# Performance work log

Hardware: AMD Instinct MI355X
Metric: run time of the kernel (lower is better)

## Reference

```python
import jax, jax.numpy as jnp
import numpy as np
import math

E = 8          # num_experts (= max_expert_num)
M = 1024       # hidden_size
H = 4096       # expert FFN dim (4*hidden)
B, S = 4, 4096 # batch, seq
CAP_FACTOR = 1.0
MIN_CAPACITY = 4


def setup_inputs() -> dict:
    key = jax.random.key(0)
    ks = jax.random.split(key, 5)
    hidden_states = jax.random.normal(ks[0], (B, S, M), dtype=jnp.float32)
    wg = jax.random.normal(ks[1], (M, E), dtype=jnp.float32) * (M ** -0.5)  # gate Linear (no bias, as in TopKGate)
    w1 = jax.random.normal(ks[2], (E, M, H), dtype=jnp.float32) * (M ** -0.5)
    b1 = jnp.zeros((E, H), dtype=jnp.float32)
    w2 = jax.random.normal(ks[3], (E, H, M), dtype=jnp.float32) * (H ** -0.5)
    b2 = jnp.zeros((E, M), dtype=jnp.float32)
    return {"hidden_states": hidden_states, "wg": wg, "w1": w1, "b1": b1, "w2": w2, "b2": b2}


def reference(hidden_states, wg, w1, b1, w2, b2):
    b, s_len, m = hidden_states.shape
    x = hidden_states.reshape(-1, m)            # [s, m], s = tokens
    s = x.shape[0]
    capacity = max(int(math.ceil(s / E * CAP_FACTOR)), MIN_CAPACITY)  # static

    # ---- top-1 gating (DeepSpeed top1gating, fp32, no jitter, no RTS) ----
    logits = x.astype(jnp.float32) @ wg          # [s, e]
    gates = jax.nn.softmax(logits, axis=1)
    idx = jnp.argmax(gates, axis=1)              # chosen expert per token
    mask1 = jax.nn.one_hot(idx, E, dtype=jnp.float32)
    exp_counts = jnp.sum(mask1, axis=0).astype(jnp.int32)
    ce = jnp.mean(mask1, axis=0)                 # fraction routed per expert (pre-drop)
    me = jnp.mean(gates, axis=0)
    l_aux = jnp.sum(me * ce) * E                 # load-balancing loss

    # position of each token within its expert's queue; drop past capacity
    locations = jnp.cumsum(mask1, axis=0) - 1.0  # [s, e]
    loc = jnp.sum(locations * mask1, axis=1).astype(jnp.int32)  # [s]
    keep = (loc < capacity).astype(jnp.float32)  # capacity drop mask
    gate_s = jnp.sum(gates * mask1, axis=1) * keep
    loc_c = jnp.clip(loc, 0, capacity - 1)

    # ---- dispatch: scatter tokens to [E, C, M] slots (equiv. to einsum('sec,sm->ecm')) ----
    dispatched = jnp.zeros((E, capacity, m), dtype=x.dtype).at[idx, loc_c].add(x * keep[:, None])

    # ---- grouped expert GEMMs (MLP with GELU) ----
    h = jax.nn.gelu(jnp.einsum('ecm,emh->ech', dispatched, w1) + b1[:, None, :])
    eout = jnp.einsum('ech,ehm->ecm', h, w2) + b2[:, None, :]

    # ---- combine: gather back and scale by gate value (dropped tokens -> 0) ----
    out = eout[idx, loc_c] * gate_s[:, None]     # [s, m]
    return out.reshape(b, s_len, m), l_aux, exp_counts
```

## Files before the change

kernel.cpp:

```cpp
#include <hip/hip_runtime.h>
#include <hip/hip_bf16.h>

#define TOKENS 16384
#define MDIM   1024
#define HDIM   4096
#define HHALF  2048
#define NEXP   8
#define CAP    2048

typedef __attribute__((ext_vector_type(8))) short bf16x8;
typedef __attribute__((ext_vector_type(4))) float f32x4;

__device__ __forceinline__ short f2bf(float x) {
  unsigned u = __float_as_uint(x);
  unsigned r = (u + 0x7fffu + ((u >> 16) & 1u)) >> 16;
  return (short)r;
}

__device__ __forceinline__ float gelu_f(float x) {
  float u = 1.5957691216057308f * (x + 0.044715f * x * x * x);
  float e = __expf(u);
  return x * (1.f - 1.f / (e + 1.f));
}

__global__ __launch_bounds__(256) void gating_kernel(
    const float* __restrict__ x, const float* __restrict__ wg,
    int* __restrict__ idx, float* __restrict__ gate,
    float* __restrict__ mepart) {
  __shared__ float me_s[NEXP];
  int tid = threadIdx.x, wid = tid >> 6, lane = tid & 63;
  if (tid < NEXP) me_s[tid] = 0.f;
  __syncthreads();
  int t = blockIdx.x * 4 + wid;
  float acc[NEXP];
#pragma unroll
  for (int e = 0; e < NEXP; e++) acc[e] = 0.f;
  const float4* xr = (const float4*)(x + (size_t)t * MDIM);
#pragma unroll
  for (int j = 0; j < 4; j++) {
    float4 xv = xr[lane * 4 + j];
    int base = lane * 16 + j * 4;
    const float* xp = &xv.x;
#pragma unroll
    for (int i = 0; i < 4; i++) {
      float xi = xp[i];
      const float4* wr = (const float4*)(wg + (size_t)(base + i) * NEXP);
      float4 w0 = wr[0], w1 = wr[1];
      acc[0] += xi * w0.x; acc[1] += xi * w0.y; acc[2] += xi * w0.z; acc[3] += xi * w0.w;
      acc[4] += xi * w1.x; acc[5] += xi * w1.y; acc[6] += xi * w1.z; acc[7] += xi * w1.w;
    }
  }
#pragma unroll
  for (int off = 32; off > 0; off >>= 1)
#pragma unroll
    for (int e = 0; e < NEXP; e++) acc[e] += __shfl_xor(acc[e], off, 64);
  if (lane == 0) {
    float mx = acc[0]; int ai = 0;
#pragma unroll
    for (int e = 1; e < NEXP; e++) if (acc[e] > mx) { mx = acc[e]; ai = e; }
    float ex[NEXP]; float se = 0.f;
#pragma unroll
    for (int e = 0; e < NEXP; e++) { ex[e] = __expf(acc[e] - mx); se += ex[e]; }
    float inv = 1.f / se;
#pragma unroll
    for (int e = 0; e < NEXP; e++) atomicAdd(&me_s[e], ex[e] * inv);
    idx[t] = ai;
    gate[t] = inv;
  }
  __syncthreads();
  if (tid < NEXP) mepart[blockIdx.x * NEXP + tid] = me_s[tid];
}

__global__ __launch_bounds__(1024) void scan_kernel(
    const int* __restrict__ idx, float* __restrict__ gate,
    int* __restrict__ s2t, int* __restrict__ counts) {
  __shared__ int wcnt[16][NEXP];
  __shared__ int base[NEXP];
  int tid = threadIdx.x, wid = tid >> 6, lane = tid & 63;
  if (tid < NEXP) base[tid] = 0;
  __syncthreads();
  for (int chunk = 0; chunk < TOKENS; chunk += 1024) {
    int i = chunk + tid;
    int e = idx[i];
    int pre = 0;
#pragma unroll
    for (int e2 = 0; e2 < NEXP; e2++) {
      unsigned long long b = __ballot(e == e2);
      if (e2 == e) pre = __popcll(b & ((1ull << lane) - 1ull));
      if (lane == 0) wcnt[wid][e2] = __popcll(b);
    }
    __syncthreads();
    int off = base[e];
    for (int w = 0; w < wid; w++) off += wcnt[w][e];
    int loc = off + pre;
    if (loc < CAP) s2t[e * CAP + loc] = i;
    else           gate[i] = 0.f;
    __syncthreads();
    if (tid < NEXP) {
      int tsum = 0;
#pragma unroll
      for (int w = 0; w < 16; w++) tsum += wcnt[w][tid];
      base[tid] += tsum;
    }
    __syncthreads();
  }
  if (tid < NEXP) counts[tid] = base[tid];
}

__global__ __launch_bounds__(256) void finalize_kernel(
    const float* __restrict__ mepart, const int* __restrict__ counts,
    float* __restrict__ out_tail, int nblocks) {
  __shared__ float red[256];
  __shared__ float me[NEXP];
  int tid = threadIdx.x;
  float s = 0.f;
  int e = tid & 7;
  for (int r = tid >> 3; r < nblocks; r += 32) s += mepart[r * NEXP + e];
  red[tid] = s;
  __syncthreads();
  if (tid < NEXP) {
    float tsum = 0.f;
    for (int i = tid; i < 256; i += 8) tsum += red[i];
    me[tid] = tsum;
  }
  __syncthreads();
  if (tid == 0) {
    float la = 0.f;
    for (int k = 0; k < NEXP; k++)
      la += (me[k] / (float)TOKENS) * ((float)counts[k] / (float)TOKENS);
    out_tail[0] = la * (float)NEXP;
  }
  if (tid < NEXP) out_tail[1 + tid] = (float)counts[tid];
}

__global__ __launch_bounds__(256) void transpose_cvt_kernel(
    const float* __restrict__ in, short* __restrict__ out, int R, int Cc) {
  __shared__ float tile[32][33];
  int e = blockIdx.z;
  const float* in_e = in + (size_t)e * R * Cc;
  short* out_e = out + (size_t)e * R * Cc;
  int r0 = blockIdx.y * 32, c0 = blockIdx.x * 32;
  int tx = threadIdx.x & 31, ty = threadIdx.x >> 5;
#pragma unroll
  for (int i = 0; i < 4; i++)
    tile[ty + i * 8][tx] = in_e[(size_t)(r0 + ty + i * 8) * Cc + c0 + tx];
  __syncthreads();
#pragma unroll
  for (int i = 0; i < 4; i++)
    out_e[(size_t)(c0 + ty + i * 8) * R + r0 + tx] = f2bf(tile[tx][ty + i * 8]);
}

__global__ __launch_bounds__(256) void dispatch_kernel(
    const float* __restrict__ x, const int* __restrict__ s2t,
    short* __restrict__ A) {
  int slot = blockIdx.x;
  int token = s2t[slot];
  short4 v;
  if (token >= 0) {
    float4 xv = ((const float4*)(x + (size_t)token * MDIM))[threadIdx.x];
    v.x = f2bf(xv.x); v.y = f2bf(xv.y); v.z = f2bf(xv.z); v.w = f2bf(xv.w);
  } else {
    v.x = 0; v.y = 0; v.z = 0; v.w = 0;
  }
  ((short4*)(A + (size_t)slot * MDIM))[threadIdx.x] = v;
}

__device__ __forceinline__ void stage_tile(const short* __restrict__ g0, int ldk,
                                           short* lds, int tid) {
  int w = tid >> 6, lane = tid & 63;
#pragma unroll
  for (int i = 0; i < 4; i++) {
    int rbase = w * 32 + i * 8;
    int r = rbase + (lane >> 3);
    int c = (lane & 7) ^ (r & 7);
    const short* g = g0 + (size_t)r * ldk + c * 8;
    short* l = lds + rbase * 64;
    __builtin_amdgcn_global_load_lds((const __attribute__((address_space(1))) void*)g,
                                     (__attribute__((address_space(3))) void*)l,
                                     16, 0, 0);
  }
}

__global__ __launch_bounds__(256) void gemm1_kernel(
    const short* __restrict__ A, const short* __restrict__ Bt,
    const float* __restrict__ b1, short* __restrict__ Hh, int p) {
  __shared__ __align__(16) short ldsA[128 * 64];
  __shared__ __align__(16) short ldsB[128 * 64];
  int e = blockIdx.z, bm = blockIdx.y, bn = blockIdx.x;
  const short* Ae = A  + ((size_t)e * CAP  + (size_t)bm * 128) * MDIM;
  const short* Be = Bt + ((size_t)e * HDIM + (size_t)(p * HHALF + bn * 128)) * MDIM;
  int tid = threadIdx.x, lane = tid & 63, w = tid >> 6;
  int wr = (w >> 1) * 64, wc = (w & 1) * 64;
  f32x4 acc[4][4];
  f32x4 zero = {0.f, 0.f, 0.f, 0.f};
#pragma unroll
  for (int a = 0; a < 4; a++)
#pragma unroll
    for (int b = 0; b < 4; b++) acc[a][b] = zero;
  for (int kt = 0; kt < MDIM; kt += 64) {
    __syncthreads();
    stage_tile(Ae + kt, MDIM, ldsA, tid);
    stage_tile(Be + kt, MDIM, ldsB, tid);
    __syncthreads();
#pragma unroll
    for (int kk = 0; kk < 2; kk++) {
      bf16x8 af[4], bfr[4];
#pragma unroll
      for (int rt = 0; rt < 4; rt++) {
        int r = wr + rt * 16 + (lane & 15);
        int c = (kk * 4 + (lane >> 4)) ^ (r & 7);
        af[rt] = *(const bf16x8*)(ldsA + r * 64 + c * 8);
      }
#pragma unroll
      for (int ct = 0; ct < 4; ct++) {
        int r = wc + ct * 16 + (lane & 15);
        int c = (kk * 4 + (lane >> 4)) ^ (r & 7);
        bfr[ct] = *(const bf16x8*)(ldsB + r * 64 + c * 8);
      }
#pragma unroll
      for (int rt = 0; rt < 4; rt++)
#pragma unroll
        for (int ct = 0; ct < 4; ct++)
          acc[rt][ct] = __builtin_amdgcn_mfma_f32_16x16x32_bf16(af[rt], bfr[ct], acc[rt][ct], 0, 0, 0);
    }
  }
  int q = lane >> 4, ln = lane & 15;
#pragma unroll
  for (int ct = 0; ct < 4; ct++) {
    int coll = bn * 128 + wc + ct * 16 + ln;
    float bias = b1[e * HDIM + p * HHALF + coll];
#pragma unroll
    for (int rt = 0; rt < 4; rt++) {
#pragma unroll
      for (int rg = 0; rg < 4; rg++) {
        int row = bm * 128 + wr + rt * 16 + q * 4 + rg;
        float v = acc[rt][ct][rg] + bias;
        Hh[((size_t)e * CAP + row) * HHALF + coll] = f2bf(gelu_f(v));
      }
    }
  }
}

__global__ __launch_bounds__(256) void gemm2_kernel(
    const short* __restrict__ Hh, const short* __restrict__ W2t,
    const float* __restrict__ b2, const int* __restrict__ s2t,
    const float* __restrict__ gate, float* __restrict__ out, int p) {
  __shared__ __align__(16) short ldsA[128 * 64];
  __shared__ __align__(16) short ldsB[128 * 64];
  int e = blockIdx.z, bm = blockIdx.y, bn = blockIdx.x;
  const short* Ae = Hh + ((size_t)e * CAP + (size_t)bm * 128) * HHALF;
  const short* Be = W2t + ((size_t)e * MDIM + (size_t)bn * 128) * HDIM + (size_t)p * HHALF;
  int tid = threadIdx.x, lane = tid & 63, w = tid >> 6;
  int wr = (w >> 1) * 64, wc = (w & 1) * 64;
  f32x4 acc[4][4];
  f32x4 zero = {0.f, 0.f, 0.f, 0.f};
#pragma unroll
  for (int a = 0; a < 4; a++)
#pragma unroll
    for (int b = 0; b < 4; b++) acc[a][b] = zero;
  for (int kt = 0; kt < HHALF; kt += 64) {
    __syncthreads();
    stage_tile(Ae + kt, HHALF, ldsA, tid);
    stage_tile(Be + kt, HDIM, ldsB, tid);
    __syncthreads();
#pragma unroll
    for (int kk = 0; kk < 2; kk++) {
      bf16x8 af[4], bfr[4];
#pragma unroll
      for (int rt = 0; rt < 4; rt++) {
        int r = wr + rt * 16 + (lane & 15);
        int c = (kk * 4 + (lane >> 4)) ^ (r & 7);
        af[rt] = *(const bf16x8*)(ldsA + r * 64 + c * 8);
      }
#pragma unroll
      for (int ct = 0; ct < 4; ct++) {
        int r = wc + ct * 16 + (lane & 15);
        int c = (kk * 4 + (lane >> 4)) ^ (r & 7);
        bfr[ct] = *(const bf16x8*)(ldsB + r * 64 + c * 8);
      }
#pragma unroll
      for (int rt = 0; rt < 4; rt++)
#pragma unroll
        for (int ct = 0; ct < 4; ct++)
          acc[rt][ct] = __builtin_amdgcn_mfma_f32_16x16x32_bf16(af[rt], bfr[ct], acc[rt][ct], 0, 0, 0);
    }
  }
  int q = lane >> 4, ln = lane & 15;
#pragma unroll
  for (int rt = 0; rt < 4; rt++) {
#pragma unroll
    for (int rg = 0; rg < 4; rg++) {
      int row = bm * 128 + wr + rt * 16 + q * 4 + rg;
      int token = s2t[e * CAP + row];
      if (token < 0) continue;
      float g = gate[token];
#pragma unroll
      for (int ct = 0; ct < 4; ct++) {
        int col = bn * 128 + wc + ct * 16 + ln;
        float v = acc[rt][ct][rg];
        size_t o = (size_t)token * MDIM + col;
        if (p == 0) out[o] = (v + b2[e * MDIM + col]) * g;
        else        out[o] += v * g;
      }
    }
  }
}

__global__ __launch_bounds__(256) void zerodrop_kernel(
    const float* __restrict__ gate, float* __restrict__ out) {
  int t = blockIdx.x;
  if (gate[t] != 0.f) return;
  float4 z = {0.f, 0.f, 0.f, 0.f};
  ((float4*)(out + (size_t)t * MDIM))[threadIdx.x] = z;
}

extern "C" void kernel_launch(void* const* d_in, const int* in_sizes, int n_in,
                              void* d_out, int out_size, void* d_ws, size_t ws_size,
                              hipStream_t stream) {
  const float* x  = (const float*)d_in[0];
  const float* wg = (const float*)d_in[1];
  const float* w1 = (const float*)d_in[2];
  const float* b1 = (const float*)d_in[3];
  const float* w2 = (const float*)d_in[4];
  const float* b2 = (const float*)d_in[5];
  float* out = (float*)d_out;

  char* ws = (char*)d_ws;
  size_t off = 0;
  auto alloc = [&](size_t n) { char* ptr = ws + off; off += (n + 255) & ~(size_t)255; return ptr; };
  short* W1t  = (short*)alloc((size_t)NEXP * MDIM * HDIM * 2);
  short* W2t  = (short*)alloc((size_t)NEXP * MDIM * HDIM * 2);
  short* Adis = (short*)alloc((size_t)NEXP * CAP * MDIM * 2);
  short* Hh   = (short*)alloc((size_t)NEXP * CAP * HHALF * 2);
  int*   idx  = (int*)  alloc(TOKENS * 4);
  float* gate = (float*)alloc(TOKENS * 4);
  int*   s2t  = (int*)  alloc(NEXP * CAP * 4);
  float* mep  = (float*)alloc((TOKENS / 4) * NEXP * 4);
  int*   cnts = (int*)  alloc(NEXP * 4);
  if (ws_size < off) return;

  hipMemsetAsync(s2t, 0xFF, NEXP * CAP * 4, stream);

  gating_kernel<<<TOKENS / 4, 256, 0, stream>>>(x, wg, idx, gate, mep);
  scan_kernel<<<1, 1024, 0, stream>>>(idx, gate, s2t, cnts);
  finalize_kernel<<<1, 256, 0, stream>>>(mep, cnts, out + (size_t)TOKENS * MDIM, TOKENS / 4);
  transpose_cvt_kernel<<<dim3(HDIM / 32, MDIM / 32, NEXP), 256, 0, stream>>>(w1, W1t, MDIM, HDIM);
  transpose_cvt_kernel<<<dim3(MDIM / 32, HDIM / 32, NEXP), 256, 0, stream>>>(w2, W2t, HDIM, MDIM);
  dispatch_kernel<<<NEXP * CAP, 256, 0, stream>>>(x, s2t, Adis);
  for (int p = 0; p < 2; p++) {
    gemm1_kernel<<<dim3(HHALF / 128, CAP / 128, NEXP), 256, 0, stream>>>(Adis, W1t, b1, Hh, p);
    gemm2_kernel<<<dim3(MDIM / 128, CAP / 128, NEXP), 256, 0, stream>>>(Hh, W2t, b2, s2t, gate, out, p);
  }
  zerodrop_kernel<<<TOKENS, 256, 0, stream>>>(gate, out);
}
```

Measured before the change: 1.017 ms.

## Fuse dispatch into gemm1 via gathered loads and split work by expert groups

The separate dispatch kernel is removed. The gating kernel now also writes a bf16 copy of x, and gemm1 gathers token rows directly through s2t pointers, using a zero row for empty slots. The two passes now split by groups of four experts instead of by halves of the hidden dim, so gemm2 runs the full K=4096 and writes out once instead of doing a read-modify-write accumulate. The costs are an extra bf16 write of all of x and gathered, less regular A loads in gemm1.

```diff
diff --git a/kernel.cpp b/kernel.cpp
--- a/kernel.cpp
+++ b/kernel.cpp
@@ -4,8 +4,8 @@
 #define TOKENS 16384
 #define MDIM   1024
 #define HDIM   4096
-#define HHALF  2048
 #define NEXP   8
+#define EGRP   4
 #define CAP    2048
 
 typedef __attribute__((ext_vector_type(8))) short bf16x8;
@@ -26,7 +26,7 @@
 __global__ __launch_bounds__(256) void gating_kernel(
     const float* __restrict__ x, const float* __restrict__ wg,
     int* __restrict__ idx, float* __restrict__ gate,
-    float* __restrict__ mepart) {
+    float* __restrict__ mepart, short* __restrict__ xb) {
   __shared__ float me_s[NEXP];
   int tid = threadIdx.x, wid = tid >> 6, lane = tid & 63;
   if (tid < NEXP) me_s[tid] = 0.f;
@@ -36,9 +36,12 @@
 #pragma unroll
   for (int e = 0; e < NEXP; e++) acc[e] = 0.f;
   const float4* xr = (const float4*)(x + (size_t)t * MDIM);
+  short* xbr = xb + (size_t)t * MDIM + lane * 16;
 #pragma unroll
   for (int j = 0; j < 4; j++) {
     float4 xv = xr[lane * 4 + j];
+    short4 bv; bv.x = f2bf(xv.x); bv.y = f2bf(xv.y); bv.z = f2bf(xv.z); bv.w = f2bf(xv.w);
+    ((short4*)(xbr))[j] = bv;
     int base = lane * 16 + j * 4;
     const float* xp = &xv.x;
 #pragma unroll
@@ -150,21 +153,6 @@
     out_e[(size_t)(c0 + ty + i * 8) * R + r0 + tx] = f2bf(tile[tx][ty + i * 8]);
 }
 
-__global__ __launch_bounds__(256) void dispatch_kernel(
-    const float* __restrict__ x, const int* __restrict__ s2t,
-    short* __restrict__ A) {
-  int slot = blockIdx.x;
-  int token = s2t[slot];
-  short4 v;
-  if (token >= 0) {
-    float4 xv = ((const float4*)(x + (size_t)token * MDIM))[threadIdx.x];
-    v.x = f2bf(xv.x); v.y = f2bf(xv.y); v.z = f2bf(xv.z); v.w = f2bf(xv.w);
-  } else {
-    v.x = 0; v.y = 0; v.z = 0; v.w = 0;
-  }
-  ((short4*)(A + (size_t)slot * MDIM))[threadIdx.x] = v;
-}
-
 __device__ __forceinline__ void stage_tile(const short* __restrict__ g0, int ldk,
                                            short* lds, int tid) {
   int w = tid >> 6, lane = tid & 63;
@@ -182,13 +170,91 @@
 }
 
 __global__ __launch_bounds__(256) void gemm1_kernel(
-    const short* __restrict__ A, const short* __restrict__ Bt,
-    const float* __restrict__ b1, short* __restrict__ Hh, int p) {
+    const short* __restrict__ xb, const int* __restrict__ s2t,
+    const short* __restrict__ W1t, const float* __restrict__ b1,
+    short* __restrict__ Hh, const short* __restrict__ zrow, int eg) {
   __shared__ __align__(16) short ldsA[128 * 64];
   __shared__ __align__(16) short ldsB[128 * 64];
-  int e = blockIdx.z, bm = blockIdx.y, bn = blockIdx.x;
-  const short* Ae = A  + ((size_t)e * CAP  + (size_t)bm * 128) * MDIM;
-  const short* Be = Bt + ((size_t)e * HDIM + (size_t)(p * HHALF + bn * 128)) * MDIM;
+  int bz = blockIdx.z, bm = blockIdx.y, bn = blockIdx.x;
+  int e_abs = eg + bz;
+  const short* Be = W1t + ((size_t)e_abs * HDIM + (size_t)bn * 128) * MDIM;
+  int tid = threadIdx.x, lane = tid & 63, w = tid >> 6;
+  const short* aptr[4];
+#pragma unroll
+  for (int i = 0; i < 4; i++) {
+    int rb = w * 32 + i * 8;
+    int r = rb + (lane >> 3);
+    int tok = s2t[e_abs * CAP + bm * 128 + r];
+    const short* basep = (tok >= 0) ? (xb + (size_t)tok * MDIM) : zrow;
+    aptr[i] = basep + (((lane & 7) ^ (r & 7)) * 8);
+  }
+  int wr = (w >> 1) * 64, wc = (w & 1) * 64;
+  f32x4 acc[4][4];
+  f32x4 zero = {0.f, 0.f, 0.f, 0.f};
+#pragma unroll
+  for (int a = 0; a < 4; a++)
+#pragma unroll
+    for (int b = 0; b < 4; b++) acc[a][b] = zero;
+  for (int kt = 0; kt < MDIM; kt += 64) {
+    __syncthreads();
+#pragma unroll
+    for (int i = 0; i < 4; i++) {
+      short* l = ldsA + (w * 32 + i * 8) * 64;
+      __builtin_amdgcn_global_load_lds((const __attribute__((address_space(1))) void*)(aptr[i] + kt),
+                                       (__attribute__((address_space(3))) void*)l,
+                                       16, 0, 0);
+    }
+    stage_tile(Be + kt, MDIM, ldsB, tid);
+    __syncthreads();
+#pragma unroll
+    for (int kk = 0; kk < 2; kk++) {
+      bf16x8 af[4], bfr[4];
+#pragma unroll
+      for (int rt = 0; rt < 4; rt++) {
+        int r = wr + rt * 16 + (lane & 15);
+        int c = (kk * 4 + (lane >> 4)) ^ (r & 7);
+        af[rt] = *(const bf16x8*)(ldsA + r * 64 + c * 8);
+      }
+#pragma unroll
+      for (int ct = 0; ct < 4; ct++) {
+        int r = wc + ct * 16 + (lane & 15);
+        int c = (kk * 4 + (lane >> 4)) ^ (r & 7);
+        bfr[ct] = *(const bf16x8*)(ldsB + r * 64 + c * 8);
+      }
+#pragma unroll
+      for (int rt = 0; rt < 4; rt++)
+#pragma unroll
+        for (int ct = 0; ct < 4; ct++)
+          acc[rt][ct] = __builtin_amdgcn_mfma_f32_16x16x32_bf16(af[rt], bfr[ct], acc[rt][ct], 0, 0, 0);
+    }
+  }
+  int q = lane >> 4, ln = lane & 15;
+#pragma unroll
+  for (int ct = 0; ct < 4; ct++) {
+    int col = bn * 128 + wc + ct * 16 + ln;
+    float bias = b1[e_abs * HDIM + col];
+#pragma unroll
+    for (int rt = 0; rt < 4; rt++) {
+#pragma unroll
+      for (int rg = 0; rg < 4; rg++) {
+        int row = bm * 128 + wr + rt * 16 + q * 4 + rg;
+        float v = acc[rt][ct][rg] + bias;
+        Hh[((size_t)bz * CAP + row) * HDIM + col] = f2bf(gelu_f(v));
+      }
+    }
+  }
+}
+
+__global__ __launch_bounds__(256) void gemm2_kernel(
+    const short* __restrict__ Hh, const short* __restrict__ W2t,
+    const float* __restrict__ b2, const int* __restrict__ s2t,
+    const float* __restrict__ gate, float* __restrict__ out, int eg) {
+  __shared__ __align__(16) short ldsA[128 * 64];
+  __shared__ __align__(16) short ldsB[128 * 64];
+  int bz = blockIdx.z, bm = blockIdx.y, bn = blockIdx.x;
+  int e_abs = eg + bz;
+  const short* Ae = Hh + ((size_t)bz * CAP + (size_t)bm * 128) * HDIM;
+  const short* Be = W2t + ((size_t)e_abs * MDIM + (size_t)bn * 128) * HDIM;
   int tid = threadIdx.x, lane = tid & 63, w = tid >> 6;
   int wr = (w >> 1) * 64, wc = (w & 1) * 64;
   f32x4 acc[4][4];
@@ -197,10 +263,10 @@
   for (int a = 0; a < 4; a++)
 #pragma unroll
     for (int b = 0; b < 4; b++) acc[a][b] = zero;
-  for (int kt = 0; kt < MDIM; kt += 64) {
-    __syncthreads();
-    stage_tile(Ae + kt, MDIM, ldsA, tid);
-    stage_tile(Be + kt, MDIM, ldsB, tid);
+  for (int kt = 0; kt < HDIM; kt += 64) {
+    __syncthreads();
+    stage_tile(Ae + kt, HDIM, ldsA, tid);
+    stage_tile(Be + kt, HDIM, ldsB, tid);
     __syncthreads();
 #pragma unroll
     for (int kk = 0; kk < 2; kk++) {
@@ -225,82 +291,21 @@
     }
   }
   int q = lane >> 4, ln = lane & 15;
-#pragma unroll
-  for (int ct = 0; ct < 4; ct++) {
-    int coll = bn * 128 + wc + ct * 16 + ln;
-    float bias = b1[e * HDIM + p * HHALF + coll];
-#pragma unroll
-    for (int rt = 0; rt < 4; rt++) {
-#pragma unroll
-      for (int rg = 0; rg < 4; rg++) {
-        int row = bm * 128 + wr + rt * 16 + q * 4 + rg;
-        float v = acc[rt][ct][rg] + bias;
-        Hh[((size_t)e * CAP + row) * HHALF + coll] = f2bf(gelu_f(v));
-      }
-    }
-  }
-}
-
-__global__ __launch_bounds__(256) void gemm2_kernel(
-    const short* __restrict__ Hh, const short* __restrict__ W2t,
-    const float* __restrict__ b2, const int* __restrict__ s2t,
-    const float* __restrict__ gate, float* __restrict__ out, int p) {
-  __shared__ __align__(16) short ldsA[128 * 64];
-  __shared__ __align__(16) short ldsB[128 * 64];
-  int e = blockIdx.z, bm = blockIdx.y, bn = blockIdx.x;
-  const short* Ae = Hh + ((size_t)e * CAP + (size_t)bm * 128) * HHALF;
-  const short* Be = W2t + ((size_t)e * MDIM + (size_t)bn * 128) * HDIM + (size_t)p * HHALF;
-  int tid = threadIdx.x, lane = tid & 63, w = tid >> 6;
-  int wr = (w >> 1) * 64, wc = (w & 1) * 64;
-  f32x4 acc[4][4];
-  f32x4 zero = {0.f, 0.f, 0.f, 0.f};
-#pragma unroll
-  for (int a = 0; a < 4; a++)
-#pragma unroll
-    for (int b = 0; b < 4; b++) acc[a][b] = zero;
-  for (int kt = 0; kt < HHALF; kt += 64) {
-    __syncthreads();
-    stage_tile(Ae + kt, HHALF, ldsA, tid);
-    stage_tile(Be + kt, HDIM, ldsB, tid);
-    __syncthreads();
-#pragma unroll
-    for (int kk = 0; kk < 2; kk++) {
-      bf16x8 af[4], bfr[4];
-#pragma unroll
-      for (int rt = 0; rt < 4; rt++) {
-        int r = wr + rt * 16 + (lane & 15);
-        int c = (kk * 4 + (lane >> 4)) ^ (r & 7);
-        af[rt] = *(const bf16x8*)(ldsA + r * 64 + c * 8);
-      }
-#pragma unroll
-      for (int ct = 0; ct < 4; ct++) {
-        int r = wc + ct * 16 + (lane & 15);
-        int c = (kk * 4 + (lane >> 4)) ^ (r & 7);
-        bfr[ct] = *(const bf16x8*)(ldsB + r * 64 + c * 8);
-      }
-#pragma unroll
-      for (int rt = 0; rt < 4; rt++)
-#pragma unroll
-        for (int ct = 0; ct < 4; ct++)
-          acc[rt][ct] = __builtin_amdgcn_mfma_f32_16x16x32_bf16(af[rt], bfr[ct], acc[rt][ct], 0, 0, 0);
-    }
-  }
-  int q = lane >> 4, ln = lane & 15;
+  float bias[4];
+#pragma unroll
+  for (int ct = 0; ct < 4; ct++) bias[ct] = b2[e_abs * MDIM + bn * 128 + wc + ct * 16 + ln];
 #pragma unroll
   for (int rt = 0; rt < 4; rt++) {
 #pragma unroll
     for (int rg = 0; rg < 4; rg++) {
       int row = bm * 128 + wr + rt * 16 + q * 4 + rg;
-      int token = s2t[e * CAP + row];
+      int token = s2t[e_abs * CAP + row];
       if (token < 0) continue;
       float g = gate[token];
 #pragma unroll
       for (int ct = 0; ct < 4; ct++) {
         int col = bn * 128 + wc + ct * 16 + ln;
-        float v = acc[rt][ct][rg];
-        size_t o = (size_t)token * MDIM + col;
-        if (p == 0) out[o] = (v + b2[e * MDIM + col]) * g;
-        else        out[o] += v * g;
+        out[(size_t)token * MDIM + col] = (acc[rt][ct][rg] + bias[ct]) * g;
       }
     }
   }
@@ -330,8 +335,9 @@
   auto alloc = [&](size_t n) { char* ptr = ws + off; off += (n + 255) & ~(size_t)255; return ptr; };
   short* W1t  = (short*)alloc((size_t)NEXP * MDIM * HDIM * 2);
   short* W2t  = (short*)alloc((size_t)NEXP * MDIM * HDIM * 2);
-  short* Adis = (short*)alloc((size_t)NEXP * CAP * MDIM * 2);
-  short* Hh   = (short*)alloc((size_t)NEXP * CAP * HHALF * 2);
+  short* Hh   = (short*)alloc((size_t)EGRP * CAP * HDIM * 2);
+  short* xb   = (short*)alloc((size_t)TOKENS * MDIM * 2);
+  short* zrow = (short*)alloc((size_t)MDIM * 2);
   int*   idx  = (int*)  alloc(TOKENS * 4);
   float* gate = (float*)alloc(TOKENS * 4);
   int*   s2t  = (int*)  alloc(NEXP * CAP * 4);
@@ -340,16 +346,16 @@
   if (ws_size < off) return;
 
   hipMemsetAsync(s2t, 0xFF, NEXP * CAP * 4, stream);
-
-  gating_kernel<<<TOKENS / 4, 256, 0, stream>>>(x, wg, idx, gate, mep);
+  hipMemsetAsync(zrow, 0, MDIM * 2, stream);
+
+  gating_kernel<<<TOKENS / 4, 256, 0, stream>>>(x, wg, idx, gate, mep, xb);
   scan_kernel<<<1, 1024, 0, stream>>>(idx, gate, s2t, cnts);
   finalize_kernel<<<1, 256, 0, stream>>>(mep, cnts, out + (size_t)TOKENS * MDIM, TOKENS / 4);
   transpose_cvt_kernel<<<dim3(HDIM / 32, MDIM / 32, NEXP), 256, 0, stream>>>(w1, W1t, MDIM, HDIM);
   transpose_cvt_kernel<<<dim3(MDIM / 32, HDIM / 32, NEXP), 256, 0, stream>>>(w2, W2t, HDIM, MDIM);
-  dispatch_kernel<<<NEXP * CAP, 256, 0, stream>>>(x, s2t, Adis);
-  for (int p = 0; p < 2; p++) {
-    gemm1_kernel<<<dim3(HHALF / 128, CAP / 128, NEXP), 256, 0, stream>>>(Adis, W1t, b1, Hh, p);
-    gemm2_kernel<<<dim3(MDIM / 128, CAP / 128, NEXP), 256, 0, stream>>>(Hh, W2t, b2, s2t, gate, out, p);
+  for (int g = 0; g < 2; g++) {
+    gemm1_kernel<<<dim3(HDIM / 128, CAP / 128, EGRP), 256, 0, stream>>>(xb, s2t, W1t, b1, Hh, zrow, g * EGRP);
+    gemm2_kernel<<<dim3(MDIM / 128, CAP / 128, EGRP), 256, 0, stream>>>(Hh, W2t, b2, s2t, gate, out, g * EGRP);
   }
   zerodrop_kernel<<<TOKENS, 256, 0, stream>>>(gate, out);
 }
```

New measurement: 933.6 us. 8.2% less time.
